# Kernel tuning notes

Measured on AMD Instinct MI355X. Metric: run time of the kernel, lower is better.

Reference implementation:

```python
import jax, jax.numpy as jnp
import numpy as np

B, N, K = 8, 4096, 5


def setup_inputs() -> dict:
    key = jax.random.key(0)
    ks = jax.random.split(key, 24)
    s = 0.05
    inp = {
        'pointcloud': jax.random.normal(ks[0], (B, 3, N, 1), jnp.float32),
        # local 1x1 conv stack (bias-free) + BN affine params (eval mode, stats=identity)
        'conv_w1': jax.random.normal(ks[1], (64, 3), jnp.float32) * s,
        'bn1_g': jnp.ones((64,), jnp.float32), 'bn1_b': jnp.zeros((64,), jnp.float32),
        'conv_w2': jax.random.normal(ks[2], (64, 64), jnp.float32) * s,
        'bn2_g': jnp.ones((64,), jnp.float32), 'bn2_b': jnp.zeros((64,), jnp.float32),
        'conv_w3': jax.random.normal(ks[3], (64, 64), jnp.float32) * s,
        'bn3_g': jnp.ones((64,), jnp.float32), 'bn3_b': jnp.zeros((64,), jnp.float32),
        'conv_w4': jax.random.normal(ks[4], (128, 64), jnp.float32) * s,
        'bn4_g': jnp.ones((128,), jnp.float32), 'bn4_b': jnp.zeros((128,), jnp.float32),
        # GCN layers
        'gc1_w': jax.random.normal(ks[5], (128, 128), jnp.float32) * s,
        'gc1_b': jnp.zeros((128,), jnp.float32),
        'gc2_w': jax.random.normal(ks[6], (128, 128), jnp.float32) * s,
        'gc2_b': jnp.zeros((128,), jnp.float32),
        'gc3_w': jax.random.normal(ks[7], (128, 256), jnp.float32) * s,
        'gc3_b': jnp.zeros((256,), jnp.float32),
        # MLP head
        'fc1_w': jax.random.normal(ks[8], (512, 256), jnp.float32) * s,
        'bnf1_g': jnp.ones((512,), jnp.float32), 'bnf1_b': jnp.zeros((512,), jnp.float32),
        'fc2_w': jax.random.normal(ks[9], (256, 512), jnp.float32) * s,
        'bnf2_g': jnp.ones((256,), jnp.float32), 'bnf2_b': jnp.zeros((256,), jnp.float32),
        'fc3_w': jax.random.normal(ks[10], (128, 256), jnp.float32) * s,
        'fc3_b': jnp.zeros((128,), jnp.float32),
    }
    return inp


def _cbr(h, w, g, b):
    # 1x1 conv (per-point linear) + BatchNorm(eval, identity stats) + ReLU
    return jax.nn.relu((h @ w.T) * g + b)


def reference(pointcloud, conv_w1, bn1_g, bn1_b, conv_w2, bn2_g, bn2_b,
              conv_w3, bn3_g, bn3_b, conv_w4, bn4_g, bn4_b,
              gc1_w, gc1_b, gc2_w, gc2_b, gc3_w, gc3_b,
              fc1_w, bnf1_g, bnf1_b, fc2_w, bnf2_g, bnf2_b, fc3_w, fc3_b):
    pts = pointcloud[..., 0]                       # [B,3,N]
    b, _, n = pts.shape

    # ---- LocalOperation: sort points by distance to centroid, gather ----
    centroid = pts.mean(axis=2, keepdims=True)     # [B,3,1]
    d_cent = ((pts - centroid) ** 2).sum(axis=1)   # [B,N]
    order = jnp.argsort(d_cent, axis=-1)           # [B,N]
    x = jnp.take_along_axis(pts, order[:, None, :], axis=2)  # [B,3,N]

    h = x.transpose(0, 2, 1)                       # [B,N,3]
    h = _cbr(h, conv_w1, bn1_g, bn1_b)             # [B,N,64]
    h = _cbr(h, conv_w2, bn2_g, bn2_b)
    h = _cbr(h, conv_w3, bn3_g, bn3_b)
    h = _cbr(h, conv_w4, bn4_g, bn4_b)             # [B,N,128]
    feat = h.reshape(b * n, 128)                   # node features

    # ---- KNN graph (k=5, within each cloud, self included like KDTree) ----
    sq = (pts ** 2).sum(axis=1)                                        # [B,N]
    d2 = sq[:, :, None] + sq[:, None, :] - 2.0 * jnp.einsum('bcn,bcm->bnm', pts, pts)
    _, nbr = jax.lax.top_k(-d2, K)                                     # [B,N,K]
    offsets = (jnp.arange(b) * n)[:, None, None]
    src = (nbr + offsets).reshape(-1)                                  # [B*N*K]
    dst = jnp.broadcast_to(jnp.arange(b * n).reshape(b, n, 1), (b, n, K)).reshape(-1)

    num_nodes = b * n
    ones = jnp.ones_like(src, jnp.float32)
    deg_out = jax.ops.segment_sum(ones, src, num_segments=num_nodes)
    deg_in = jax.ops.segment_sum(ones, dst, num_segments=num_nodes)
    norm_out = jax.lax.rsqrt(jnp.maximum(deg_out, 1.0))
    norm_in = jax.lax.rsqrt(jnp.maximum(deg_in, 1.0))

    def gcn(hh, w, bias):
        hw = (hh @ w) * norm_out[:, None]          # [BN,F] pre-normed features
        msg = hw[src]                              # gather
        agg = jax.ops.segment_sum(msg, dst, num_segments=num_nodes)  # scatter-add
        return agg * norm_in[:, None] + bias

    g = jax.nn.relu(gcn(feat, gc1_w, gc1_b))       # [BN,128]
    g = jax.nn.relu(gcn(g, gc2_w, gc2_b))          # [BN,128]
    g = gcn(g, gc3_w, gc3_b)                       # [BN,256]

    # ---- head (BN eval, dropout eval = identity) ----
    z = jax.nn.relu((g @ fc1_w.T) * bnf1_g + bnf1_b)   # [BN,512]
    z = jax.nn.relu((z @ fc2_w.T) * bnf2_g + bnf2_b)   # [BN,256]
    pooled = z.max(axis=0)                             # [256] global max over nodes
    out = pooled @ fc3_w.T + fc3_b                     # [128]
    return out
```

## Files before the change

kernel.cpp:

```cpp
#include <hip/hip_runtime.h>
#include <math.h>
#include <float.h>

#define NB 8
#define NP 4096
#define BN_ (NB*NP)
#define KNN 5
#define JCH 512
#define NJC (NP/JCH)
#define SENT 64

typedef unsigned short u16;
typedef __attribute__((ext_vector_type(8))) __bf16 bf16x8;
typedef __attribute__((ext_vector_type(4))) float f32x4;

__device__ __forceinline__ u16 f2bf(float x){
  unsigned u = __float_as_uint(x);
  u += 0x7fff + ((u>>16)&1);
  return (u16)(u>>16);
}
__device__ __forceinline__ float bf2f(u16 h){ return __uint_as_float(((unsigned)h)<<16); }


__global__ void k_centroid(const float* __restrict__ pc, float* __restrict__ dcent,
                           int* __restrict__ rankb) {
  int b = blockIdx.x, tid = threadIdx.x;
  const float* px = pc + (size_t)b*3*NP;
  const float* py = px + NP;
  const float* pz = py + NP;
  double sx=0, sy=0, sz=0;
  for (int n = tid; n < NP; n += 256) { sx += px[n]; sy += py[n]; sz += pz[n]; }
  __shared__ double rx[256], ry[256], rz[256];
  rx[tid]=sx; ry[tid]=sy; rz[tid]=sz;
  __syncthreads();
  for (int s = 128; s > 0; s >>= 1) {
    if (tid < s) { rx[tid]+=rx[tid+s]; ry[tid]+=ry[tid+s]; rz[tid]+=rz[tid+s]; }
    __syncthreads();
  }
  __shared__ float cxs, cys, czs;
  if (tid == 0) {
    cxs = (float)(rx[0]/NP); cys = (float)(ry[0]/NP); czs = (float)(rz[0]/NP);
  }
  __syncthreads();
  float cx = cxs, cy = cys, cz = czs;
  for (int n = tid; n < NP; n += 256) {
    float dx = __fsub_rn(px[n], cx);
    float dy = __fsub_rn(py[n], cy);
    float dz = __fsub_rn(pz[n], cz);
    float d = __fadd_rn(__fadd_rn(__fmul_rn(dx,dx), __fmul_rn(dy,dy)), __fmul_rn(dz,dz));
    dcent[b*NP + n] = d;
    rankb[b*NP + n] = 0;
  }
}

__global__ void __launch_bounds__(256) k_rank_part(const float* __restrict__ dcent,
                                                   int* __restrict__ rank) {
  int jc = blockIdx.x, ic = blockIdx.y, b = blockIdx.z;
  __shared__ float d[JCH];
  int j0 = jc*JCH;
  for (int n = threadIdx.x; n < JCH; n += 256) d[n] = dcent[b*NP + j0 + n];
  __syncthreads();
  int i = ic*256 + threadIdx.x;
  float di = dcent[b*NP + i];
  int cnt = 0;
  #pragma unroll 8
  for (int n = 0; n < JCH; ++n) {
    float dj = d[n];
    cnt += (dj < di) || (dj == di && (j0 + n) < i);
  }
  atomicAdd(&rank[b*NP + i], cnt);
}

__global__ void k_scatprep(const float* __restrict__ pc, const int* __restrict__ rank,
                           const float* __restrict__ dcent,
                           int* __restrict__ ord, float4* __restrict__ srt,
                           float* __restrict__ rcv, int* __restrict__ deg) {
  int idx = blockIdx.x*256 + threadIdx.x;
  int b = idx >> 12, i = idx & (NP-1);
  int r = rank[idx];
  ord[b*NP + r] = i;
  const float* base = pc + (size_t)b*3*NP;
  float x = base[i], y = base[NP+i], z = base[2*NP+i];
  float sq = __fadd_rn(__fadd_rn(__fmul_rn(x,x), __fmul_rn(y,y)), __fmul_rn(z,z));
  float4 v; v.x=x; v.y=y; v.z=z; v.w=sq;
  srt[b*NP + r] = v;
  rcv[b*NP + r] = sqrtf(dcent[idx]);
  deg[idx] = 0;
}

#define INS(dist, q) \
  if (dist < b4) { \
    if (dist < b3) { b4=b3; r4=r3; \
      if (dist < b2) { b3=b2; r3=r2; \
        if (dist < b1) { b2=b1; r2=r1; \
          if (dist < b0) { b1=b0; r1=r0; b0=dist; r0=(q); } \
          else { b1=dist; r1=(q); } \
        } else { b2=dist; r2=(q); } \
      } else { b3=dist; r3=(q); } \
    } else { b4=dist; r4=(q); } \
  }

__global__ void __launch_bounds__(512) k_knn_ann4(const float4* __restrict__ srt,
                                                  const float* __restrict__ rc,
                                                  const int* __restrict__ ord,
                                                  int* __restrict__ nbr,
                                                  int* __restrict__ deg) {
  __shared__ float4 tile[NP + 2*SENT];
  int b = blockIdx.x >> 6;
  int blk = blockIdx.x & 63;
  int gbase = b*NP;
  for (int t = threadIdx.x; t < NP + 2*SENT; t += 512) {
    int q = t - SENT;
    if ((unsigned)q < NP) tile[t] = srt[gbase + q];
    else { float4 s4; s4.x=0.f; s4.y=0.f; s4.z=0.f; s4.w=1e30f; tile[t] = s4; }
  }
  __syncthreads();

  const int lane = threadIdx.x & 63;
  const int wv   = threadIdx.x >> 6;
  const int grp  = lane >> 3;
  const int sub  = lane & 7;
  const int s_i  = blk*64 + wv*8 + grp;

  float4 p = tile[SENT + s_i];
  float xi=p.x, yi=p.y, zi=p.z, sqi=p.w;
  float ri = rc[gbase + s_i];

  const bool is_hi = (sub < 4);
  const int step = is_hi ? 4 : -4;
  const int jdead = is_hi ? (NP + 7) : (-36);
  int j = is_hi ? (s_i + sub) : (s_i - 1 - (sub - 4));
  bool alive = ((unsigned)j < NP);
  if (!alive) j = jdead;

  float b0=FLT_MAX, b1=FLT_MAX, b2=FLT_MAX, b3=FLT_MAX, b4=FLT_MAX;
  int r0=0, r1=0, r2=0, r3=0, r4=0;

  while (__ballot(alive)) {
    float4 jp[8];
    #pragma unroll
    for (int t = 0; t < 8; ++t) jp[t] = tile[SENT + j + step*t];
    #pragma unroll
    for (int t = 0; t < 8; ++t) {
      float dot = __fadd_rn(__fadd_rn(__fmul_rn(xi,jp[t].x), __fmul_rn(yi,jp[t].y)), __fmul_rn(zi,jp[t].z));
      float dist = __fsub_rn(__fadd_rn(sqi, jp[t].w), __fmul_rn(2.0f, dot));
      if (__ballot(dist < b4)) { INS(dist, j + step*t) }
    }
    float bm = b4;
    bm = fminf(bm, __shfl_xor(bm, 1));
    bm = fminf(bm, __shfl_xor(bm, 2));
    bm = fminf(bm, __shfl_xor(bm, 4));
    float T = bm*1.0002f + 1e-9f;
    int qe = j + step*7;
    qe = qe < 0 ? 0 : (qe > NP-1 ? NP-1 : qe);
    float dr = fabsf(ri - rc[gbase + qe]);
    bool nextin = ((unsigned)(j + step*8) < NP);
    alive = alive && nextin && (__fmul_rn(dr,dr) < T);
    j = alive ? (j + step*8) : jdead;
  }

  #pragma unroll
  for (int m = 1; m <= 4; m <<= 1) {
    float c0=__shfl_xor(b0,m), c1=__shfl_xor(b1,m), c2=__shfl_xor(b2,m),
          c3=__shfl_xor(b3,m), c4=__shfl_xor(b4,m);
    int   s0=__shfl_xor(r0,m), s1=__shfl_xor(r1,m), s2=__shfl_xor(r2,m),
          s3=__shfl_xor(r3,m), s4=__shfl_xor(r4,m);
    if (c0 < b4) { INS(c0, s0)
      if (c1 < b4) { INS(c1, s1)
        if (c2 < b4) { INS(c2, s2)
          if (c3 < b4) { INS(c3, s3)
            if (c4 < b4) { INS(c4, s4) }
          }
        }
      }
    }
  }

  if (sub == 0) {
    int oi = ord[gbase + s_i];
    int node = gbase + oi;
    int nb = node*KNN;
    int o0 = gbase + ord[gbase+r0], o1 = gbase + ord[gbase+r1], o2 = gbase + ord[gbase+r2];
    int o3 = gbase + ord[gbase+r3], o4 = gbase + ord[gbase+r4];
    nbr[nb+0]=o0; nbr[nb+1]=o1; nbr[nb+2]=o2; nbr[nb+3]=o3; nbr[nb+4]=o4;
    atomicAdd(&deg[o0],1); atomicAdd(&deg[o1],1); atomicAdd(&deg[o2],1);
    atomicAdd(&deg[o3],1); atomicAdd(&deg[o4],1);
  }
}

__global__ void k_cvt_all(const float* __restrict__ w2, const float* __restrict__ w3,
                          const float* __restrict__ w4, const float* __restrict__ gc1,
                          const float* __restrict__ gc2, const float* __restrict__ gc3,
                          const float* __restrict__ fc1, const float* __restrict__ fc2,
                          u16* o2, u16* o3, u16* o4, u16* og1, u16* og2, u16* og3,
                          u16* of1, u16* of2) {
  int i = blockIdx.x*256 + threadIdx.x;
  if (i < 4096) { o2[i] = f2bf(w2[i]); return; } i -= 4096;
  if (i < 4096) { o3[i] = f2bf(w3[i]); return; } i -= 4096;
  if (i < 8192) { o4[i] = f2bf(w4[i]); return; } i -= 8192;
  if (i < 16384) { int n=i>>7, k=i&127; og1[i] = f2bf(gc1[k*128+n]); return; } i -= 16384;
  if (i < 16384) { int n=i>>7, k=i&127; og2[i] = f2bf(gc2[k*128+n]); return; } i -= 16384;
  if (i < 32768) { int n=i>>7, k=i&127; og3[i] = f2bf(gc3[k*256+n]); return; } i -= 32768;
  if (i < 131072) { of1[i] = f2bf(fc1[i]); return; } i -= 131072;
  if (i < 131072) { of2[i] = f2bf(fc2[i]); }
}

__global__ void k_conv1(const float* __restrict__ pc, const int* __restrict__ ord,
                        const float* __restrict__ w, const float* __restrict__ g,
                        const float* __restrict__ bias, u16* __restrict__ outp,
                        float* __restrict__ pooled) {
  if (blockIdx.x == 0) pooled[threadIdx.x] = 0.0f;
  int node = blockIdx.x*4 + (threadIdx.x >> 6);
  int o = threadIdx.x & 63;
  int b = node >> 12;
  int j = ord[node];
  const float* base = pc + (size_t)b*3*NP;
  float x = base[j], y = base[NP + j], z = base[2*NP + j];
  float acc = x*w[o*3+0] + y*w[o*3+1] + z*w[o*3+2];
  float v = fmaxf(acc*g[o] + bias[o], 0.0f);
  outp[(size_t)node*64 + o] = f2bf(v);
}

template<int BNT>
__global__ __launch_bounds__(256) void gemm_bf16(
    const u16* __restrict__ A, const u16* __restrict__ W,
    const float* __restrict__ gamma, const float* __restrict__ beta,
    const int* __restrict__ degp, void* __restrict__ Cout,
    int K, int Nc, int mode) {
  constexpr int NF = BNT/32;
  __shared__ u16 As[128*64];
  __shared__ u16 Bs[BNT*64];
  const int tid = threadIdx.x;
  const int w = tid >> 6, l = tid & 63;
  const int m0 = blockIdx.x*128, n0 = blockIdx.y*BNT;
  const int wm = w & 1, wn = w >> 1;
  const int lr = l >> 3;
  const int lc = l & 7;
  const int fm = l & 15, fk = l >> 4;

  f32x4 acc[4][NF];
  #pragma unroll
  for (int i=0;i<4;++i)
    #pragma unroll
    for (int j=0;j<NF;++j) acc[i][j] = (f32x4){0.f,0.f,0.f,0.f};

  for (int k0 = 0; k0 < K; k0 += 64) {
    #pragma unroll
    for (int t=0;t<4;++t){
      int row = (w*4 + t)*8 + lr;
      uint4 v = *(const uint4*)(A + ((size_t)(m0+row)*K + k0 + lc*8));
      *(uint4*)&As[row*64 + ((lc ^ (row&7))*8)] = v;
    }
    #pragma unroll
    for (int t=0;t<NF;++t){
      int row = (w*NF + t)*8 + lr;
      uint4 v = *(const uint4*)(W + ((size_t)(n0+row)*K + k0 + lc*8));
      *(uint4*)&Bs[row*64 + ((lc ^ (row&7))*8)] = v;
    }
    __syncthreads();
    #pragma unroll
    for (int ks=0; ks<2; ++ks){
      bf16x8 af[4], bfr[NF];
      #pragma unroll
      for (int mf=0; mf<4; ++mf){
        int row = wm*64 + mf*16 + fm;
        int ck = ks*4 + fk;
        af[mf] = *(const bf16x8*)&As[row*64 + ((ck ^ (row&7))*8)];
      }
      #pragma unroll
      for (int nf=0; nf<NF; ++nf){
        int row = wn*(BNT/2) + nf*16 + fm;
        int ck = ks*4 + fk;
        bfr[nf] = *(const bf16x8*)&Bs[row*64 + ((ck ^ (row&7))*8)];
      }
      #pragma unroll
      for (int mf=0; mf<4; ++mf)
        #pragma unroll
        for (int nf=0; nf<NF; ++nf)
          acc[mf][nf] = __builtin_amdgcn_mfma_f32_16x16x32_bf16(af[mf], bfr[nf], acc[mf][nf], 0, 0, 0);
    }
    __syncthreads();
  }

  const int col_base = n0 + wn*(BNT/2);
  if (mode == 1) {
    u16* C = (u16*)Cout;
    #pragma unroll
    for (int mf=0; mf<4; ++mf){
      #pragma unroll
      for (int r=0;r<4;++r){
        int row = m0 + wm*64 + mf*16 + fk*4 + r;
        int d = degp[row]; if (d < 1) d = 1;
        float rs = 1.0f / sqrtf((float)d);
        #pragma unroll
        for (int nf=0;nf<NF;++nf){
          int col = col_base + nf*16 + fm;
          C[(size_t)row*Nc + col] = f2bf(acc[mf][nf][r]*rs);
        }
      }
    }
  } else if (mode == 3) {
    unsigned int* pool = (unsigned int*)Cout;
    float gv[NF], bv[NF], cm[NF];
    #pragma unroll
    for (int nf=0;nf<NF;++nf){
      int col = col_base + nf*16 + fm;
      gv[nf] = gamma[col]; bv[nf] = beta[col];
      cm[nf] = 0.0f;
    }
    #pragma unroll
    for (int mf=0; mf<4; ++mf)
      #pragma unroll
      for (int r=0;r<4;++r)
        #pragma unroll
        for (int nf=0;nf<NF;++nf){
          float v = fmaxf(acc[mf][nf][r]*gv[nf] + bv[nf], 0.f);
          cm[nf] = fmaxf(cm[nf], v);
        }
    #pragma unroll
    for (int nf=0;nf<NF;++nf){
      float m = cm[nf];
      m = fmaxf(m, __shfl_xor(m, 16));
      m = fmaxf(m, __shfl_xor(m, 32));
      if (fk == 0)
        atomicMax(&pool[col_base + nf*16 + fm], __float_as_uint(m));
    }
  } else {
    float gv[NF], bv[NF];
    #pragma unroll
    for (int nf=0;nf<NF;++nf){
      int col = col_base + nf*16 + fm;
      gv[nf] = gamma[col]; bv[nf] = beta[col];
    }
    #pragma unroll
    for (int mf=0; mf<4; ++mf){
      #pragma unroll
      for (int r=0;r<4;++r){
        int row = m0 + wm*64 + mf*16 + fk*4 + r;
        #pragma unroll
        for (int nf=0;nf<NF;++nf){
          int col = col_base + nf*16 + fm;
          float v = fmaxf(acc[mf][nf][r]*gv[nf] + bv[nf], 0.f);
          ((u16*)Cout)[(size_t)row*Nc + col] = f2bf(v);
        }
      }
    }
  }
}

__global__ void k_agg_bf(const u16* __restrict__ hw, const int* __restrict__ nbr,
                         const float* __restrict__ bias, u16* __restrict__ outp,
                         int F, int do_relu) {
  int per = F >> 3;
  int gid = blockIdx.x*256 + threadIdx.x;
  int i = gid / per;
  int f = (gid - i*per) * 8;
  const int* nb = nbr + i*KNN;
  float s[8] = {0,0,0,0,0,0,0,0};
  #pragma unroll
  for (int k = 0; k < KNN; ++k) {
    uint4 v = *(const uint4*)(hw + (size_t)nb[k]*F + f);
    const u16* h = (const u16*)&v;
    #pragma unroll
    for (int j=0;j<8;++j) s[j] += bf2f(h[j]);
  }
  const float ninv = 0.44721359549995793f;
  u16 o[8];
  #pragma unroll
  for (int j=0;j<8;++j){
    float v = s[j]*ninv + bias[f+j];
    if (do_relu) v = fmaxf(v, 0.f);
    o[j] = f2bf(v);
  }
  *(uint4*)&outp[(size_t)i*F + f] = *(const uint4*)o;
}

__global__ void k_fc3(const float* __restrict__ pooled, const float* __restrict__ w,
                      const float* __restrict__ bias, float* __restrict__ outp) {
  __shared__ float p[256];
  int tid = threadIdx.x;
  p[tid] = pooled[tid];
  p[tid + 128] = pooled[tid + 128];
  __syncthreads();
  float s = 0.0f;
  for (int i = 0; i < 256; ++i) s = fmaf(w[tid*256 + i], p[i], s);
  outp[tid] = s + bias[tid];
}

extern "C" void kernel_launch(void* const* d_in, const int* in_sizes, int n_in,
                              void* d_out, int out_size, void* d_ws, size_t ws_size,
                              hipStream_t stream) {
  const float* pc   = (const float*)d_in[0];
  const float* w1   = (const float*)d_in[1];
  const float* g1   = (const float*)d_in[2];
  const float* b1   = (const float*)d_in[3];
  const float* w2   = (const float*)d_in[4];
  const float* g2   = (const float*)d_in[5];
  const float* b2   = (const float*)d_in[6];
  const float* w3   = (const float*)d_in[7];
  const float* g3   = (const float*)d_in[8];
  const float* b3   = (const float*)d_in[9];
  const float* w4   = (const float*)d_in[10];
  const float* g4   = (const float*)d_in[11];
  const float* b4   = (const float*)d_in[12];
  const float* gc1w = (const float*)d_in[13];
  const float* gc1b = (const float*)d_in[14];
  const float* gc2w = (const float*)d_in[15];
  const float* gc2b = (const float*)d_in[16];
  const float* gc3w = (const float*)d_in[17];
  const float* gc3b = (const float*)d_in[18];
  const float* fc1w = (const float*)d_in[19];
  const float* f1g  = (const float*)d_in[20];
  const float* f1b  = (const float*)d_in[21];
  const float* fc2w = (const float*)d_in[22];
  const float* f2g  = (const float*)d_in[23];
  const float* f2b  = (const float*)d_in[24];
  const float* fc3w = (const float*)d_in[25];
  const float* fc3b = (const float*)d_in[26];
  float* outp = (float*)d_out;

  char* wsb = (char*)d_ws;
  size_t off = 0;
  auto alloc = [&](size_t bytes) -> void* {
    void* p = wsb + off;
    off += (bytes + 255) & ~(size_t)255;
    return p;
  };
  int*   ord    = (int*)  alloc((size_t)BN_*4);
  int*   deg    = (int*)  alloc((size_t)BN_*4);
  int*   rankb  = (int*)  alloc((size_t)BN_*4);
  int*   nbr    = (int*)  alloc((size_t)BN_*KNN*4);
  float* dcent  = (float*)alloc((size_t)BN_*4);
  float* pooled = (float*)alloc(256*4);
  float4* srt   = (float4*)alloc((size_t)BN_*16);
  float* rc     = (float*)alloc((size_t)BN_*4);
  u16* wb2   = (u16*)alloc(64*64*2);
  u16* wb3   = (u16*)alloc(64*64*2);
  u16* wb4   = (u16*)alloc(128*64*2);
  u16* wgc1  = (u16*)alloc(128*128*2);
  u16* wgc2  = (u16*)alloc(128*128*2);
  u16* wgc3  = (u16*)alloc(256*128*2);
  u16* wfc1  = (u16*)alloc(512*256*2);
  u16* wfc2  = (u16*)alloc(256*512*2);
  u16* h1   = (u16*)alloc((size_t)BN_*64*2);
  u16* h2   = (u16*)alloc((size_t)BN_*64*2);
  u16* feat = (u16*)alloc((size_t)BN_*128*2);
  u16* hw   = (u16*)alloc((size_t)BN_*256*2);
  u16* gb1  = (u16*)alloc((size_t)BN_*128*2);
  u16* g3b  = (u16*)alloc((size_t)BN_*256*2);
  u16* z1   = (u16*)alloc((size_t)BN_*512*2);

  k_cvt_all<<<1344, 256, 0, stream>>>(w2, w3, w4, gc1w, gc2w, gc3w, fc1w, fc2w,
                                      wb2, wb3, wb4, wgc1, wgc2, wgc3, wfc1, wfc2);

  k_centroid<<<NB, 256, 0, stream>>>(pc, dcent, rankb);
  k_rank_part<<<dim3(NJC, NP/256, NB), 256, 0, stream>>>(dcent, rankb);
  k_scatprep<<<BN_/256, 256, 0, stream>>>(pc, rankb, dcent, ord, srt, rc, deg);
  k_knn_ann4<<<NB*64, 512, 0, stream>>>(srt, rc, ord, nbr, deg);

  k_conv1<<<BN_/4, 256, 0, stream>>>(pc, ord, w1, g1, b1, h1, pooled);
  gemm_bf16<64><<<dim3(BN_/128, 1), 256, 0, stream>>>(h1, wb2, g2, b2, nullptr, h2, 64, 64, 0);
  gemm_bf16<64><<<dim3(BN_/128, 1), 256, 0, stream>>>(h2, wb3, g3, b3, nullptr, h1, 64, 64, 0);
  gemm_bf16<128><<<dim3(BN_/128, 1), 256, 0, stream>>>(h1, wb4, g4, b4, nullptr, feat, 64, 128, 0);

  gemm_bf16<128><<<dim3(BN_/128, 1), 256, 0, stream>>>(feat, wgc1, nullptr, nullptr, deg, hw, 128, 128, 1);
  k_agg_bf<<<(BN_*16)/256, 256, 0, stream>>>(hw, nbr, gc1b, gb1, 128, 1);
  gemm_bf16<128><<<dim3(BN_/128, 1), 256, 0, stream>>>(gb1, wgc2, nullptr, nullptr, deg, hw, 128, 128, 1);
  k_agg_bf<<<(BN_*16)/256, 256, 0, stream>>>(hw, nbr, gc2b, feat, 128, 1);
  gemm_bf16<128><<<dim3(BN_/128, 2), 256, 0, stream>>>(feat, wgc3, nullptr, nullptr, deg, hw, 128, 256, 1);
  k_agg_bf<<<(BN_*32)/256, 256, 0, stream>>>(hw, nbr, gc3b, g3b, 256, 0);

  gemm_bf16<128><<<dim3(BN_/128, 4), 256, 0, stream>>>(g3b, wfc1, f1g, f1b, nullptr, z1, 256, 512, 0);
  gemm_bf16<128><<<dim3(BN_/128, 2), 256, 0, stream>>>(z1, wfc2, f2g, f2b, nullptr, pooled, 512, 256, 3);
  k_fc3<<<1, 128, 0, stream>>>(pooled, fc3w, fc3b, outp);
}
```

Measured before the change: 341.4 us.

## Fuse local conv stack into one kernel keeping activations in LDS

```diff
diff --git a/kernel.cpp b/kernel.cpp
--- a/kernel.cpp
+++ b/kernel.cpp
@@ -205,20 +205,178 @@
   if (i < 131072) { of2[i] = f2bf(fc2[i]); }
 }
 
-__global__ void k_conv1(const float* __restrict__ pc, const int* __restrict__ ord,
-                        const float* __restrict__ w, const float* __restrict__ g,
-                        const float* __restrict__ bias, u16* __restrict__ outp,
-                        float* __restrict__ pooled) {
-  if (blockIdx.x == 0) pooled[threadIdx.x] = 0.0f;
-  int node = blockIdx.x*4 + (threadIdx.x >> 6);
-  int o = threadIdx.x & 63;
-  int b = node >> 12;
-  int j = ord[node];
-  const float* base = pc + (size_t)b*3*NP;
-  float x = base[j], y = base[NP + j], z = base[2*NP + j];
-  float acc = x*w[o*3+0] + y*w[o*3+1] + z*w[o*3+2];
-  float v = fmaxf(acc*g[o] + bias[o], 0.0f);
-  outp[(size_t)node*64 + o] = f2bf(v);
+__global__ void __launch_bounds__(256) k_convstack(
+    const float* __restrict__ pc, const int* __restrict__ ord,
+    const float* __restrict__ w1, const float* __restrict__ g1, const float* __restrict__ b1,
+    const u16* __restrict__ wb2, const float* __restrict__ g2, const float* __restrict__ b2,
+    const u16* __restrict__ wb3, const float* __restrict__ g3, const float* __restrict__ b3,
+    const u16* __restrict__ wb4, const float* __restrict__ g4, const float* __restrict__ b4,
+    u16* __restrict__ feat, float* __restrict__ pooled) {
+  __shared__ float xs[128], ys[128], zs[128];
+  __shared__ u16 hA[128*64];
+  __shared__ u16 hB[128*64];
+  __shared__ u16 wbuf[128*64];
+  const int tid = threadIdx.x;
+  const int m0 = blockIdx.x * 128;
+  const int b = m0 >> 12;
+  if (blockIdx.x == 0) pooled[tid] = 0.0f;
+  if (tid < 128) {
+    int j = ord[m0 + tid];
+    const float* base = pc + (size_t)b*3*NP;
+    xs[tid] = base[j]; ys[tid] = base[NP + j]; zs[tid] = base[2*NP + j];
+  }
+  #pragma unroll
+  for (int it = 0; it < 2; ++it) {
+    int t = tid + it*256;
+    int row = t >> 3, lc = t & 7;
+    uint4 v = *(const uint4*)(wb2 + ((size_t)row*64 + lc*8));
+    *(uint4*)&wbuf[row*64 + ((lc ^ (row&7))*8)] = v;
+  }
+  __syncthreads();
+
+  for (int idx = tid; idx < 128*64; idx += 256) {
+    int n = idx >> 6, o = idx & 63;
+    float x = xs[n], y = ys[n], z = zs[n];
+    float acc = x*w1[o*3+0] + y*w1[o*3+1] + z*w1[o*3+2];
+    float v = fmaxf(acc*g1[o] + b1[o], 0.0f);
+    hA[n*64 + (((o>>3) ^ (n&7))*8) + (o&7)] = f2bf(v);
+  }
+  __syncthreads();
+
+  const int w = tid >> 6, l = tid & 63;
+  const int wm = w & 1, wn = w >> 1;
+  const int fm = l & 15, fk = l >> 4;
+
+  {
+    f32x4 acc[4][2];
+    #pragma unroll
+    for (int i=0;i<4;++i) { acc[i][0]=(f32x4){0,0,0,0}; acc[i][1]=(f32x4){0,0,0,0}; }
+    #pragma unroll
+    for (int ks=0; ks<2; ++ks){
+      bf16x8 af[4], bfr[2];
+      #pragma unroll
+      for (int mf=0; mf<4; ++mf){
+        int row = wm*64 + mf*16 + fm; int ck = ks*4 + fk;
+        af[mf] = *(const bf16x8*)&hA[row*64 + ((ck ^ (row&7))*8)];
+      }
+      #pragma unroll
+      for (int nf=0; nf<2; ++nf){
+        int row = wn*32 + nf*16 + fm; int ck = ks*4 + fk;
+        bfr[nf] = *(const bf16x8*)&wbuf[row*64 + ((ck ^ (row&7))*8)];
+      }
+      #pragma unroll
+      for (int mf=0; mf<4; ++mf)
+        #pragma unroll
+        for (int nf=0; nf<2; ++nf)
+          acc[mf][nf] = __builtin_amdgcn_mfma_f32_16x16x32_bf16(af[mf], bfr[nf], acc[mf][nf], 0, 0, 0);
+    }
+    #pragma unroll
+    for (int mf=0; mf<4; ++mf)
+      #pragma unroll
+      for (int r=0;r<4;++r){
+        int row = wm*64 + mf*16 + fk*4 + r;
+        #pragma unroll
+        for (int nf=0;nf<2;++nf){
+          int col = wn*32 + nf*16 + fm;
+          float v = fmaxf(acc[mf][nf][r]*g2[col] + b2[col], 0.f);
+          hB[row*64 + (((col>>3) ^ (row&7))*8) + (col&7)] = f2bf(v);
+        }
+      }
+  }
+  __syncthreads();
+  #pragma unroll
+  for (int it = 0; it < 2; ++it) {
+    int t = tid + it*256;
+    int row = t >> 3, lc = t & 7;
+    uint4 v = *(const uint4*)(wb3 + ((size_t)row*64 + lc*8));
+    *(uint4*)&wbuf[row*64 + ((lc ^ (row&7))*8)] = v;
+  }
+  __syncthreads();
+
+  {
+    f32x4 acc[4][2];
+    #pragma unroll
+    for (int i=0;i<4;++i) { acc[i][0]=(f32x4){0,0,0,0}; acc[i][1]=(f32x4){0,0,0,0}; }
+    #pragma unroll
+    for (int ks=0; ks<2; ++ks){
+      bf16x8 af[4], bfr[2];
+      #pragma unroll
+      for (int mf=0; mf<4; ++mf){
+        int row = wm*64 + mf*16 + fm; int ck = ks*4 + fk;
+        af[mf] = *(const bf16x8*)&hB[row*64 + ((ck ^ (row&7))*8)];
+      }
+      #pragma unroll
+      for (int nf=0; nf<2; ++nf){
+        int row = wn*32 + nf*16 + fm; int ck = ks*4 + fk;
+        bfr[nf] = *(const bf16x8*)&wbuf[row*64 + ((ck ^ (row&7))*8)];
+      }
+      #pragma unroll
+      for (int mf=0; mf<4; ++mf)
+        #pragma unroll
+        for (int nf=0; nf<2; ++nf)
+          acc[mf][nf] = __builtin_amdgcn_mfma_f32_16x16x32_bf16(af[mf], bfr[nf], acc[mf][nf], 0, 0, 0);
+    }
+    #pragma unroll
+    for (int mf=0; mf<4; ++mf)
+      #pragma unroll
+      for (int r=0;r<4;++r){
+        int row = wm*64 + mf*16 + fk*4 + r;
+        #pragma unroll
+        for (int nf=0;nf<2;++nf){
+          int col = wn*32 + nf*16 + fm;
+          float v = fmaxf(acc[mf][nf][r]*g3[col] + b3[col], 0.f);
+          hA[row*64 + (((col>>3) ^ (row&7))*8) + (col&7)] = f2bf(v);
+        }
+      }
+  }
+  __syncthreads();
+  #pragma unroll
+  for (int it = 0; it < 4; ++it) {
+    int t = tid + it*256;
+    int row = t >> 3, lc = t & 7;
+    uint4 v = *(const uint4*)(wb4 + ((size_t)row*64 + lc*8));
+    *(uint4*)&wbuf[row*64 + ((lc ^ (row&7))*8)] = v;
+  }
+  __syncthreads();
+
+  {
+    f32x4 acc[4][4];
+    #pragma unroll
+    for (int i=0;i<4;++i)
+      #pragma unroll
+      for (int jn=0;jn<4;++jn) acc[i][jn]=(f32x4){0,0,0,0};
+    #pragma unroll
+    for (int ks=0; ks<2; ++ks){
+      bf16x8 af[4], bfr[4];
+      #pragma unroll
+      for (int mf=0; mf<4; ++mf){
+        int row = wm*64 + mf*16 + fm; int ck = ks*4 + fk;
+        af[mf] = *(const bf16x8*)&hA[row*64 + ((ck ^ (row&7))*8)];
+      }
+      #pragma unroll
+      for (int nf=0; nf<4; ++nf){
+        int row = wn*64 + nf*16 + fm; int ck = ks*4 + fk;
+        bfr[nf] = *(const bf16x8*)&wbuf[row*64 + ((ck ^ (row&7))*8)];
+      }
+      #pragma unroll
+      for (int mf=0; mf<4; ++mf)
+        #pragma unroll
+        for (int nf=0; nf<4; ++nf)
+          acc[mf][nf] = __builtin_amdgcn_mfma_f32_16x16x32_bf16(af[mf], bfr[nf], acc[mf][nf], 0, 0, 0);
+    }
+    #pragma unroll
+    for (int mf=0; mf<4; ++mf)
+      #pragma unroll
+      for (int r=0;r<4;++r){
+        int row = m0 + wm*64 + mf*16 + fk*4 + r;
+        #pragma unroll
+        for (int nf=0;nf<4;++nf){
+          int col = wn*64 + nf*16 + fm;
+          float v = fmaxf(acc[mf][nf][r]*g4[col] + b4[col], 0.f);
+          feat[(size_t)row*128 + col] = f2bf(v);
+        }
+      }
+  }
 }
 
 template<int BNT>
@@ -442,8 +600,6 @@
   u16* wgc3  = (u16*)alloc(256*128*2);
   u16* wfc1  = (u16*)alloc(512*256*2);
   u16* wfc2  = (u16*)alloc(256*512*2);
-  u16* h1   = (u16*)alloc((size_t)BN_*64*2);
-  u16* h2   = (u16*)alloc((size_t)BN_*64*2);
   u16* feat = (u16*)alloc((size_t)BN_*128*2);
   u16* hw   = (u16*)alloc((size_t)BN_*256*2);
   u16* gb1  = (u16*)alloc((size_t)BN_*128*2);
@@ -458,10 +614,9 @@
   k_scatprep<<<BN_/256, 256, 0, stream>>>(pc, rankb, dcent, ord, srt, rc, deg);
   k_knn_ann4<<<NB*64, 512, 0, stream>>>(srt, rc, ord, nbr, deg);
 
-  k_conv1<<<BN_/4, 256, 0, stream>>>(pc, ord, w1, g1, b1, h1, pooled);
-  gemm_bf16<64><<<dim3(BN_/128, 1), 256, 0, stream>>>(h1, wb2, g2, b2, nullptr, h2, 64, 64, 0);
-  gemm_bf16<64><<<dim3(BN_/128, 1), 256, 0, stream>>>(h2, wb3, g3, b3, nullptr, h1, 64, 64, 0);
-  gemm_bf16<128><<<dim3(BN_/128, 1), 256, 0, stream>>>(h1, wb4, g4, b4, nullptr, feat, 64, 128, 0);
+  k_convstack<<<BN_/128, 256, 0, stream>>>(pc, ord, w1, g1, b1,
+                                           wb2, g2, b2, wb3, g3, b3, wb4, g4, b4,
+                                           feat, pooled);
 
   gemm_bf16<128><<<dim3(BN_/128, 1), 256, 0, stream>>>(feat, wgc1, nullptr, nullptr, deg, hw, 128, 128, 1);
   k_agg_bf<<<(BN_*16)/256, 256, 0, stream>>>(hw, nbr, gc1b, gb1, 128, 1);
```

Result: no change. 338.6 us (-0.8%).
